# Kernel optimization log

Hardware: AMD Instinct MI355X
Metric: run time of the kernel (lower is better)

Reference implementation:

```python
import jax, jax.numpy as jnp
import numpy as np

B, S, D = 4, 2048, 1024  # batch, seq_len (= context_length), d_in = d_out


def setup_inputs() -> dict:
    key = jax.random.key(0)
    k0, k1, k2, k3 = jax.random.split(key, 4)
    scale = 1.0 / np.sqrt(D)  # keep activations well-scaled
    return {
        "x": jax.random.normal(k0, (B, S, D), dtype=jnp.float32),
        "Wq": jax.random.normal(k1, (D, D), dtype=jnp.float32) * scale,
        "Wk": jax.random.normal(k2, (D, D), dtype=jnp.float32) * scale,
        "Wv": jax.random.normal(k3, (D, D), dtype=jnp.float32) * scale,
    }


def reference(x, Wq, Wk, Wv):
    # Linear projections (torch Linear with bias=False == x @ W^T; here weights
    # are stored pre-transposed as [d_in, d_out]).
    q = jnp.einsum("bsd,de->bse", x, Wq)
    k = jnp.einsum("bsd,de->bse", x, Wk)
    v = jnp.einsum("bsd,de->bse", x, Wv)

    d_k = k.shape[-1]
    scores = jnp.einsum("bqd,bkd->bqk", q, k) / jnp.sqrt(jnp.float32(d_k))

    # Causal mask: disallow attending to future tokens (strict upper triangle).
    n = x.shape[1]
    causal = jnp.tril(jnp.ones((n, n), dtype=bool))  # True = allowed
    scores = jnp.where(causal[None, :, :], scores, -jnp.inf)

    attn = jax.nn.softmax(scores, axis=-1)
    # dropout_ratio = 0.0 -> identity (eval-mode equivalent)
    return jnp.einsum("bqk,bkd->bqd", attn, v)
```

## Files before the change

### kernel.cpp

```cpp
#include <hip/hip_runtime.h>
#include <math.h>


typedef float  f32x4  __attribute__((ext_vector_type(4)));
typedef int    i32x4  __attribute__((ext_vector_type(4)));
typedef __bf16 bf16x8 __attribute__((ext_vector_type(8)));

__device__ inline ushort f2bf(float f) {
    union { float f; unsigned u; } a; a.f = f;
    unsigned u = a.u;
    return (ushort)((u + 0x7fffu + ((u >> 16) & 1u)) >> 16);
}
__device__ inline bf16x8 as_bf(i32x4 v) {
    union { i32x4 i; bf16x8 b; } u; u.i = v; return u.b;
}

#define GLDS(gp, lp)                                                         \
    __builtin_amdgcn_global_load_lds(                                        \
        (const __attribute__((address_space(1))) void*)(gp),                 \
        (__attribute__((address_space(3))) void*)(lp), 16, 0, 0)

#define BKK 32

__device__ inline int swz(int row, int c) { return c ^ ((row >> 1) & 3); }

template <int BMT, int BNT, int MODE, int OUT>
__global__ __launch_bounds__((BMT / 64) * (BNT / 64) * 64,
                             ((BMT / 64) * (BNT / 64) == 8) ? 4 : 3)
void gemm_bf16(
    const ushort* __restrict__ A, const ushort* __restrict__ B0,
    float* __restrict__ Cf, ushort* __restrict__ Cb, ushort* __restrict__ Vt,
    int N, int K, int lda, int ldb,
    long long sA, long long sB, long long sC, float alpha)
{
    constexpr int NWC = BNT / 64;
    constexpr int T   = (BMT / 64) * NWC * 64;
    constexpr int RPG = T / 4;
    constexpr int IA  = BMT / RPG;
    constexpr int IB  = BNT / RPG;
    constexpr int L   = IA + IB;
    static_assert(L == 3 || L == 4, "gate literals cover L=3,4");

    __shared__ ushort SH[3 * BMT * BKK + 3 * BNT * BKK];
#define ASB(bi) (SH + (bi) * (BMT * BKK))
#define BSB(bi) (SH + 3 * (BMT * BKK) + (bi) * (BNT * BKK))

    A  += (long long)blockIdx.z * sA;
    B0 += (long long)blockIdx.z * sB;

    int bx = blockIdx.x, byi = blockIdx.y;
    {
        const int nwg = (int)(gridDim.x * gridDim.y);
        int flat = byi * (int)gridDim.x + bx;
        flat = (flat & 7) * (nwg >> 3) + (flat >> 3);
        bx  = flat % (int)gridDim.x;
        byi = flat / (int)gridDim.x;
    }
    if (MODE != 0) byi = (int)gridDim.y - 1 - byi;

    const int m0 = byi * BMT;
    const int n0 = bx * BNT;
    if (MODE == 1 && n0 > m0 + (BMT - 1)) return;
    int kend = K;
    if (MODE == 2) kend = min(K, m0 + BMT);

    const int tid = threadIdx.x;
    const int l   = tid & 63;
    const int w   = tid >> 6;
    const int g   = l >> 4;
    const int r16 = l & 15;
    const int wr  = w / NWC, wc = w % NWC;

    f32x4 acc[4][4];
#pragma unroll
    for (int mi = 0; mi < 4; ++mi)
#pragma unroll
        for (int ni = 0; ni < 4; ++ni)
            acc[mi][ni] = (f32x4){0.f, 0.f, 0.f, 0.f};

    const int srow = w * 16 + (l >> 2);
    const int cg   = swz(srow, l & 3);
    const ushort* gA = A  + (size_t)(m0 + srow) * lda + cg * 8;
    const ushort* gB = B0 + (size_t)(n0 + srow) * ldb + cg * 8;

#define STAGE(bi, k0)                                                        \
    do {                                                                     \
        _Pragma("unroll")                                                    \
        for (int ia = 0; ia < IA; ++ia)                                      \
            GLDS(gA + (k0) + (size_t)(ia * RPG) * lda,                       \
                 ASB(bi) + (ia * RPG + w * 16) * BKK);                       \
        _Pragma("unroll")                                                    \
        for (int ib = 0; ib < IB; ++ib)                                      \
            GLDS(gB + (k0) + (size_t)(ib * RPG) * ldb,                       \
                 BSB(bi) + (ib * RPG + w * 16) * BKK);                       \
    } while (0)

    const int nt = kend / BKK;
    STAGE(0, 0);
    if (nt > 1) STAGE(1, BKK);

    int cur = 0;
    for (int t = 0; t < nt; ++t) {
        if (t + 1 < nt) {
            if constexpr (L == 3)
                asm volatile("s_waitcnt vmcnt(3)" ::: "memory");
            else
                asm volatile("s_waitcnt vmcnt(4)" ::: "memory");
        } else {
            asm volatile("s_waitcnt vmcnt(0)" ::: "memory");
        }
        __builtin_amdgcn_s_barrier();
        asm volatile("" ::: "memory");

        const int nxt = (cur >= 1) ? cur - 1 : 2;
        if (t + 2 < nt) STAGE(nxt, (t + 2) * BKK);

        const ushort* Ab = ASB(cur);
        const ushort* Bb = BSB(cur);
        i32x4 av[4], bv[4];
#pragma unroll
        for (int mi = 0; mi < 4; ++mi) {
            const int r = wr * 64 + mi * 16 + r16;
            av[mi] = *(const i32x4*)(Ab + r * BKK + swz(r, g) * 8);
        }
#pragma unroll
        for (int ni = 0; ni < 4; ++ni) {
            const int r = wc * 64 + ni * 16 + r16;
            bv[ni] = *(const i32x4*)(Bb + r * BKK + swz(r, g) * 8);
        }

        __builtin_amdgcn_s_setprio(1);
#pragma unroll
        for (int mi = 0; mi < 4; ++mi)
#pragma unroll
            for (int ni = 0; ni < 4; ++ni)
                acc[mi][ni] = __builtin_amdgcn_mfma_f32_16x16x32_bf16(
                    as_bf(av[mi]), as_bf(bv[ni]), acc[mi][ni], 0, 0, 0);
        __builtin_amdgcn_s_setprio(0);

        asm volatile("" ::: "memory");
        cur = (cur == 2) ? 0 : cur + 1;
    }
#undef STAGE

    if constexpr (OUT == 1) {
        if (n0 >= 2048) {
            ushort* Tb = SH;
            __builtin_amdgcn_s_barrier();
            asm volatile("" ::: "memory");
#pragma unroll
            for (int mi = 0; mi < 4; ++mi) {
#pragma unroll
                for (int ni = 0; ni < 4; ++ni) {
                    const int c0 = wc * 64 + ni * 16 + r16;
                    const int r0 = wr * 64 + mi * 16 + g * 4;
                    ushort4 pk;
                    pk.x = f2bf(acc[mi][ni][0]);
                    pk.y = f2bf(acc[mi][ni][1]);
                    pk.z = f2bf(acc[mi][ni][2]);
                    pk.w = f2bf(acc[mi][ni][3]);
                    *(ushort4*)&Tb[c0 * 136 + r0] = pk;
                }
            }
            asm volatile("" ::: "memory");
            __builtin_amdgcn_s_barrier();
            asm volatile("" ::: "memory");

            const int bb = m0 >> 11, s0 = m0 & 2047;
            const int dl = tid >> 4;
            const int sc = (tid & 15) * 8;
#pragma unroll
            for (int p = 0; p < 8; ++p) {
                const int d = p * 32 + dl;
                const i32x4 v = *(const i32x4*)&Tb[d * 136 + sc];
                *(i32x4*)(Vt + (size_t)bb * 2097152
                          + (size_t)(n0 - 2048 + d) * 2048 + s0 + sc) = v;
            }
            return;
        }
#pragma unroll
        for (int mi = 0; mi < 4; ++mi)
#pragma unroll
            for (int ni = 0; ni < 4; ++ni)
#pragma unroll
                for (int rr = 0; rr < 4; ++rr) {
                    const int gr = m0 + wr * 64 + mi * 16 + g * 4 + rr;
                    const int gc = n0 + wc * 64 + ni * 16 + r16;
                    Cb[(size_t)gr * N + gc] = f2bf(acc[mi][ni][rr]);
                }
        return;
    }

#pragma unroll
    for (int mi = 0; mi < 4; ++mi)
#pragma unroll
        for (int ni = 0; ni < 4; ++ni)
#pragma unroll
            for (int rr = 0; rr < 4; ++rr) {
                const int gr = m0 + wr * 64 + mi * 16 + g * 4 + rr;
                const int gc = n0 + wc * 64 + ni * 16 + r16;
                Cf[(long long)blockIdx.z * sC + (size_t)gr * N + gc] =
                    acc[mi][ni][rr] * alpha;
            }
#undef ASB
#undef BSB
}

__global__ __launch_bounds__(256) void softmax_bf16(float* __restrict__ Sc)
{
    const int row = blockIdx.x;
    float* base = Sc + ((size_t)blockIdx.y * 2048 + row) * 2048;
    const int tid = threadIdx.x;
    const int j0  = tid * 8;
    const int wv  = tid >> 6;

    float s[8];
    if (j0 <= row) {
        const float4 a = *(const float4*)(base + j0);
        const float4 b = *(const float4*)(base + j0 + 4);
        s[0] = a.x; s[1] = a.y; s[2] = a.z; s[3] = a.w;
        s[4] = b.x; s[5] = b.y; s[6] = b.z; s[7] = b.w;
#pragma unroll
        for (int i = 0; i < 8; ++i)
            if (j0 + i > row) s[i] = -INFINITY;
    } else {
#pragma unroll
        for (int i = 0; i < 8; ++i) s[i] = -INFINITY;
    }

    __shared__ float rm[4], rs[4];

    float m = -INFINITY;
#pragma unroll
    for (int i = 0; i < 8; ++i) m = fmaxf(m, s[i]);
#pragma unroll
    for (int o = 32; o > 0; o >>= 1) m = fmaxf(m, __shfl_xor(m, o));
    if ((tid & 63) == 0) rm[wv] = m;
    __syncthreads();
    m = fmaxf(fmaxf(rm[0], rm[1]), fmaxf(rm[2], rm[3]));

    float e[8], sum = 0.f;
#pragma unroll
    for (int i = 0; i < 8; ++i) {
        e[i] = (j0 + i <= row) ? __expf(s[i] - m) : 0.f;
        sum += e[i];
    }
#pragma unroll
    for (int o = 32; o > 0; o >>= 1) sum += __shfl_xor(sum, o);
    if ((tid & 63) == 0) rs[wv] = sum;
    __syncthreads();
    const float inv = 1.f / (rs[0] + rs[1] + rs[2] + rs[3]);

    const int wcols = ((row >> 7) + 1) << 7;
    if (j0 < wcols) {
        i32x4 pk;
        pk[0] = (int)((unsigned)f2bf(e[0] * inv) | ((unsigned)f2bf(e[1] * inv) << 16));
        pk[1] = (int)((unsigned)f2bf(e[2] * inv) | ((unsigned)f2bf(e[3] * inv) << 16));
        pk[2] = (int)((unsigned)f2bf(e[4] * inv) | ((unsigned)f2bf(e[5] * inv) << 16));
        pk[3] = (int)((unsigned)f2bf(e[6] * inv) | ((unsigned)f2bf(e[7] * inv) << 16));
        *(i32x4*)((ushort*)base + j0) = pk;
    }
}

__global__ __launch_bounds__(256) void cvt_all(
    const float4* __restrict__ x4, ushort4* __restrict__ xb4,
    const float* __restrict__ Wq, const float* __restrict__ Wk,
    const float* __restrict__ Wv, ushort* __restrict__ Wt3)
{
    const int b = blockIdx.x;
    if (b < 8192) {
        const int i = b * 256 + threadIdx.x;
        const float4 f = x4[i];
        ushort4 u;
        u.x = f2bf(f.x); u.y = f2bf(f.y); u.z = f2bf(f.z); u.w = f2bf(f.w);
        xb4[i] = u;
        return;
    }
    const int t  = b - 8192;
    const int z  = t >> 10;
    const int r  = t & 1023;
    const int bxw = r & 31, byw = r >> 5;

    const float* W = (z == 0) ? Wq : (z == 1) ? Wk : Wv;
    ushort* Wt = Wt3 + (size_t)z * 1048576;

    __shared__ float tle[32][33];
    const int tx = threadIdx.x & 31, ty = threadIdx.x >> 5;
    const int c = bxw * 32 + tx;
    const int rbase = byw * 32;
#pragma unroll
    for (int i = 0; i < 4; ++i)
        tle[ty + i * 8][tx] = W[(size_t)(rbase + ty + i * 8) * 1024 + c];
    __syncthreads();
    const int kT = byw * 32 + tx;
    const int nT = bxw * 32;
#pragma unroll
    for (int i = 0; i < 4; ++i)
        Wt[(size_t)(nT + ty + i * 8) * 1024 + kT] = f2bf(tle[tx][ty + i * 8]);
}

extern "C" void kernel_launch(void* const* d_in, const int* in_sizes, int n_in,
                              void* d_out, int out_size, void* d_ws, size_t ws_size,
                              hipStream_t stream)
{
    (void)in_sizes; (void)n_in; (void)out_size; (void)ws_size;

    const float* x  = (const float*)d_in[0];
    const float* Wq = (const float*)d_in[1];
    const float* Wk = (const float*)d_in[2];
    const float* Wv = (const float*)d_in[3];
    float* out = (float*)d_out;

    const int NB = 4, S = 2048, D = 1024;
    const long long SD  = (long long)S * D;
    const long long NSD = NB * SD;
    const long long SS  = (long long)S * S;

    ushort* xb   = (ushort*)d_ws;
    ushort* Wt3  = xb   + NSD;
    ushort* QKVb = Wt3  + 3 * (size_t)D * D;
    ushort* Vt   = QKVb + (size_t)NB * S * 3 * D;
    float*  Sc   = (float*)(Vt + NSD);

    dim3 blk(256), blk5(512);

    cvt_all<<<dim3(8192 + 3072), blk, 0, stream>>>(
        (const float4*)x, (ushort4*)xb, Wq, Wk, Wv, Wt3);

    dim3 gp(3 * D / 256, (unsigned)(NB * S / 128), 1);
    gemm_bf16<128, 256, 0, 1><<<gp, blk5, 0, stream>>>(
        xb, Wt3, nullptr, QKVb, Vt,
        3 * D, D, D, D, 0, 0, 0, 1.f);

    dim3 gs(S / 256, S / 128, NB);
    gemm_bf16<128, 256, 1, 0><<<gs, blk5, 0, stream>>>(
        QKVb, QKVb + 1024, Sc, nullptr, nullptr,
        S, D, 3 * D, 3 * D, (long long)S * 3 * D, (long long)S * 3 * D,
        SS, 0.03125f);

    softmax_bf16<<<dim3(S, NB), blk, 0, stream>>>(Sc);

    dim3 gv(D / 256, S / 128, NB);
    gemm_bf16<128, 256, 2, 0><<<gv, blk5, 0, stream>>>(
        (const ushort*)Sc, Vt, out, nullptr, nullptr,
        D, S, 2 * S, S, 2 * SS, SD, SD, 1.f);
}
```

Before: 158.8 us.

## Split-K the causal PV GEMM for lower rows to balance work

The P·V GEMM for query rows at or beyond 1024 is split along the key dimension. One block computes keys [0,1024) and writes into the output, and a second block computes keys [1024,end) into a float partial buffer that reuses the bf16 x workspace. A new add_partial kernel then sums the partial into the output. This evens out the causal triangle's load imbalance, where bottom-row blocks had twice the K-length, at the cost of an extra launch and an extra read-modify-write of half the output. The row reversal that used to order heavy blocks first is also dropped for this mode.

```diff
diff --git a/kernel.cpp b/kernel.cpp
--- a/kernel.cpp
+++ b/kernel.cpp
@@ -30,6 +30,7 @@
 void gemm_bf16(
     const ushort* __restrict__ A, const ushort* __restrict__ B0,
     float* __restrict__ Cf, ushort* __restrict__ Cb, ushort* __restrict__ Vt,
+    float* __restrict__ Pf,
     int N, int K, int lda, int ldb,
     long long sA, long long sB, long long sC, float alpha)
 {
@@ -56,13 +57,19 @@
         bx  = flat % (int)gridDim.x;
         byi = flat / (int)gridDim.x;
     }
-    if (MODE != 0) byi = (int)gridDim.y - 1 - byi;
-
-    const int m0 = byi * BMT;
+    if (MODE == 1) byi = (int)gridDim.y - 1 - byi;
+
+    int m0, kbeg = 0, kend = K;
+    if (MODE == 2 && byi >= 16) {
+        m0 = (byi - 8) * BMT;
+        kbeg = 1024;
+        kend = m0 + BMT;
+    } else {
+        m0 = byi * BMT;
+        if (MODE == 2) kend = min(m0 + BMT, 1024);
+    }
     const int n0 = bx * BNT;
     if (MODE == 1 && n0 > m0 + (BMT - 1)) return;
-    int kend = K;
-    if (MODE == 2) kend = min(K, m0 + BMT);
 
     const int tid = threadIdx.x;
     const int l   = tid & 63;
@@ -95,9 +102,9 @@
                  BSB(bi) + (ib * RPG + w * 16) * BKK);                       \
     } while (0)
 
-    const int nt = kend / BKK;
-    STAGE(0, 0);
-    if (nt > 1) STAGE(1, BKK);
+    const int nt = (kend - kbeg) / BKK;
+    STAGE(0, kbeg);
+    if (nt > 1) STAGE(1, kbeg + BKK);
 
     int cur = 0;
     for (int t = 0; t < nt; ++t) {
@@ -113,7 +120,7 @@
         asm volatile("" ::: "memory");
 
         const int nxt = (cur >= 1) ? cur - 1 : 2;
-        if (t + 2 < nt) STAGE(nxt, (t + 2) * BKK);
+        if (t + 2 < nt) STAGE(nxt, kbeg + (t + 2) * BKK);
 
         const ushort* Ab = ASB(cur);
         const ushort* Bb = BSB(cur);
@@ -191,6 +198,20 @@
         return;
     }
 
+    if (MODE == 2 && kbeg > 0) {
+#pragma unroll
+        for (int mi = 0; mi < 4; ++mi)
+#pragma unroll
+            for (int ni = 0; ni < 4; ++ni)
+#pragma unroll
+                for (int rr = 0; rr < 4; ++rr) {
+                    const int gr = m0 + wr * 64 + mi * 16 + g * 4 + rr;
+                    const int gc = n0 + wc * 64 + ni * 16 + r16;
+                    Pf[(long long)blockIdx.z * 1048576
+                       + (size_t)(gr - 1024) * 1024 + gc] = acc[mi][ni][rr];
+                }
+        return;
+    }
 #pragma unroll
     for (int mi = 0; mi < 4; ++mi)
 #pragma unroll
@@ -206,6 +227,18 @@
 #undef BSB
 }
 
+__global__ __launch_bounds__(256) void add_partial(
+    float4* __restrict__ out4, const float4* __restrict__ Pp4)
+{
+    const int idx = blockIdx.x * 256 + threadIdx.x;
+    const int b = idx >> 18;
+    const int r = idx & 262143;
+    float4 o = out4[(size_t)b * 524288 + 262144 + r];
+    const float4 p = Pp4[idx];
+    o.x += p.x; o.y += p.y; o.z += p.z; o.w += p.w;
+    out4[(size_t)b * 524288 + 262144 + r] = o;
+}
+
 __global__ __launch_bounds__(256) void softmax_bf16(float* __restrict__ Sc)
 {
     const int row = blockIdx.x;
@@ -321,6 +354,7 @@
     ushort* QKVb = Wt3  + 3 * (size_t)D * D;
     ushort* Vt   = QKVb + (size_t)NB * S * 3 * D;
     float*  Sc   = (float*)(Vt + NSD);
+    float*  Pp   = (float*)xb;
 
     dim3 blk(256), blk5(512);
 
@@ -329,19 +363,21 @@
 
     dim3 gp(3 * D / 256, (unsigned)(NB * S / 128), 1);
     gemm_bf16<128, 256, 0, 1><<<gp, blk5, 0, stream>>>(
-        xb, Wt3, nullptr, QKVb, Vt,
+        xb, Wt3, nullptr, QKVb, Vt, nullptr,
         3 * D, D, D, D, 0, 0, 0, 1.f);
 
     dim3 gs(S / 256, S / 128, NB);
     gemm_bf16<128, 256, 1, 0><<<gs, blk5, 0, stream>>>(
-        QKVb, QKVb + 1024, Sc, nullptr, nullptr,
+        QKVb, QKVb + 1024, Sc, nullptr, nullptr, nullptr,
         S, D, 3 * D, 3 * D, (long long)S * 3 * D, (long long)S * 3 * D,
         SS, 0.03125f);
 
     softmax_bf16<<<dim3(S, NB), blk, 0, stream>>>(Sc);
 
-    dim3 gv(D / 256, S / 128, NB);
+    dim3 gv(D / 256, 24, NB);
     gemm_bf16<128, 256, 2, 0><<<gv, blk5, 0, stream>>>(
-        (const ushort*)Sc, Vt, out, nullptr, nullptr,
+        (const ushort*)Sc, Vt, out, nullptr, nullptr, Pp,
         D, S, 2 * S, S, 2 * SS, SD, SD, 1.f);
-}
+
+    add_partial<<<dim3(4096), blk, 0, stream>>>((float4*)out, (const float4*)Pp);
+}
```

After: 165.6 us. +4.3%, slower.
